# Kernel tuning notes

Hardware: AMD Instinct MI355X
Metric: run time of the kernel (lower is better)

The kernel has to match this reference:

```python
import jax, jax.numpy as jnp
import numpy as np

B, T, C, D = 4, 2048, 1024, 64

def setup_inputs() -> dict:
    key = jax.random.key(0)
    ks = jax.random.split(key, 7)
    s = 1.0 / np.sqrt(C)
    return {
        "x":  jax.random.normal(ks[0], (B, T, C), dtype=jnp.float32),
        "Wq": jax.random.uniform(ks[1], (C, D), jnp.float32, -s, s),
        "bq": jax.random.uniform(ks[2], (D,),  jnp.float32, -s, s),
        "Wk": jax.random.uniform(ks[3], (C, D), jnp.float32, -s, s),
        "bk": jax.random.uniform(ks[4], (D,),  jnp.float32, -s, s),
        "Wv": jax.random.uniform(ks[5], (C, D), jnp.float32, -s, s),
        "bv": jax.random.uniform(ks[6], (D,),  jnp.float32, -s, s),
    }

def reference(x, Wq, bq, Wk, bk, Wv, bv):
    # QKV projections: [B,T,C] @ [C,D] -> [B,T,D]
    Q = jnp.einsum('btc,cd->btd', x, Wq) + bq
    K = jnp.einsum('btc,cd->btd', x, Wk) + bk
    V = jnp.einsum('btc,cd->btd', x, Wv) + bv
    scale = 1.0 / jnp.sqrt(jnp.float32(D))
    wei = jnp.einsum('bqd,bkd->bqk', Q, K) * scale  # [B,T,T]
    causal = jnp.tril(jnp.ones((T, T), dtype=bool))
    wei = jnp.where(causal, wei, jnp.float32(-1e9))  # masked_fill, not -inf
    wei = jax.nn.softmax(wei, axis=-1)
    return jnp.einsum('bqk,bkd->bqd', wei, V)  # [B,T,D]
```

## Files before the change

kernel.cpp:

```cpp
#include <hip/hip_runtime.h>
#include <stdint.h>

#define B_  4
#define T_  2048
#define C_  1024
#define D_  64

typedef float  f32x4  __attribute__((ext_vector_type(4)));
typedef float  f32x16 __attribute__((ext_vector_type(16)));
typedef short  s16x8  __attribute__((ext_vector_type(8)));

#define QSCALE 0.18033688011112042f

static __device__ __forceinline__ uint32_t f2bf(float f) {
  uint32_t u = __builtin_bit_cast(uint32_t, f);
  u += 0x7FFFu + ((u >> 16) & 1u);
  return u >> 16;
}
static __device__ __forceinline__ uint32_t pack2bf(float a, float b) {
  return f2bf(a) | (f2bf(b) << 16);
}

__global__ __launch_bounds__(256) void wconv_kernel(
    const float* __restrict__ Wq, const float* __restrict__ bq,
    const float* __restrict__ Wk, const float* __restrict__ bk,
    const float* __restrict__ Wv, const float* __restrict__ bv,
    uint16_t* __restrict__ Wp, float* __restrict__ biascat) {
  const int g = blockIdx.x * 256 + threadIdx.x;
  const int s32   = g / 768;
  const int rem   = g - s32 * 768;
  const int ntile = rem >> 6;
  const int l     = rem & 63;
  const int mrow  = l & 15, u = l >> 4;
  const int n     = ntile * 16 + mrow;
  const int mat   = n >> 6, col = n & 63;
  const float* W  = (mat == 0) ? Wq : ((mat == 1) ? Wk : Wv);
  const float  s  = (mat == 0) ? QSCALE : 1.0f;
  const int c0    = s32 * 32 + u * 8;
  float v[8];
#pragma unroll
  for (int j = 0; j < 8; ++j) v[j] = W[(size_t)(c0 + j) * D_ + col] * s;
  uint4 st;
  st.x = pack2bf(v[0], v[1]);
  st.y = pack2bf(v[2], v[3]);
  st.z = pack2bf(v[4], v[5]);
  st.w = pack2bf(v[6], v[7]);
  *reinterpret_cast<uint4*>(Wp + (size_t)g * 8) = st;
  if (g < 192) {
    float bb;
    if (g < 64)       bb = bq[g] * QSCALE;
    else if (g < 128) bb = bk[g - 64];
    else              bb = bv[g - 128];
    biascat[g] = bb;
  }
}

__global__ __launch_bounds__(256) void proj_kernel(
    const float* __restrict__ x, const uint16_t* __restrict__ Wp,
    const float* __restrict__ biascat,
    uint16_t* __restrict__ Qfrag, uint16_t* __restrict__ Kfrag,
    uint16_t* __restrict__ Vfrag) {
  __shared__ __align__(16) uint16_t xt[2][16 * 132];
  __shared__ __align__(16) uint16_t tbuf[4][16 * 28];
  const int tid  = threadIdx.x;
  const int wave = tid >> 6;
  const int lane = tid & 63;
  const int mrow = lane & 15;
  const int u    = lane >> 4;
  const int m0   = blockIdx.x * 16;
  const int srow = tid >> 4, scol = tid & 15;

  const float* xg = x + (size_t)(m0 + srow) * C_ + scol * 4;

  f32x4 acc[3];
#pragma unroll
  for (int i = 0; i < 3; ++i)
#pragma unroll
    for (int r = 0; r < 4; ++r) acc[i][r] = 0.f;

  float4 xv0 = *reinterpret_cast<const float4*>(xg);
  float4 xv1 = *reinterpret_cast<const float4*>(xg + 64);
  {
    uint2 w0, w1;
    w0.x = pack2bf(xv0.x, xv0.y);  w0.y = pack2bf(xv0.z, xv0.w);
    w1.x = pack2bf(xv1.x, xv1.y);  w1.y = pack2bf(xv1.z, xv1.w);
    *reinterpret_cast<uint2*>(&xt[0][srow * 132 + scol * 4])      = w0;
    *reinterpret_cast<uint2*>(&xt[0][srow * 132 + scol * 4 + 64]) = w1;
  }
  __syncthreads();

  for (int s = 0; s < 8; ++s) {
    const int cur = s & 1;
    if (s < 7) {
      xv0 = *reinterpret_cast<const float4*>(xg + (s + 1) * 128);
      xv1 = *reinterpret_cast<const float4*>(xg + (s + 1) * 128 + 64);
    }
#pragma unroll
    for (int step = 0; step < 4; ++step) {
      const int s32 = s * 4 + step;
      s16x8 bf = *reinterpret_cast<const s16x8*>(
          &xt[cur][mrow * 132 + step * 32 + u * 8]);
      const uint16_t* wb = Wp + ((size_t)(s32 * 12 + wave * 3) * 64 + lane) * 8;
      s16x8 a0 = *reinterpret_cast<const s16x8*>(wb);
      s16x8 a1 = *reinterpret_cast<const s16x8*>(wb + 64 * 8);
      s16x8 a2 = *reinterpret_cast<const s16x8*>(wb + 128 * 8);
      acc[0] = __builtin_amdgcn_mfma_f32_16x16x32_bf16(a0, bf, acc[0], 0, 0, 0);
      acc[1] = __builtin_amdgcn_mfma_f32_16x16x32_bf16(a1, bf, acc[1], 0, 0, 0);
      acc[2] = __builtin_amdgcn_mfma_f32_16x16x32_bf16(a2, bf, acc[2], 0, 0, 0);
    }
    if (s < 7) {
      uint2 w0, w1;
      w0.x = pack2bf(xv0.x, xv0.y);  w0.y = pack2bf(xv0.z, xv0.w);
      w1.x = pack2bf(xv1.x, xv1.y);  w1.y = pack2bf(xv1.z, xv1.w);
      *reinterpret_cast<uint2*>(&xt[cur ^ 1][srow * 132 + scol * 4])      = w0;
      *reinterpret_cast<uint2*>(&xt[cur ^ 1][srow * 132 + scol * 4 + 64]) = w1;
      __syncthreads();
    }
  }

  const int bb  = m0 >> 11;
  const int mm  = m0 & (T_ - 1);
#pragma unroll
  for (int nt = 0; nt < 3; ++nt) {
    const int nb = wave * 48 + nt * 16;
    uint16_t vals[4];
#pragma unroll
    for (int r = 0; r < 4; ++r)
      vals[r] = (uint16_t)f2bf(acc[nt][r] + biascat[nb + u * 4 + r]);
    if (nb >= 128) {
      const int tg  = mm + mrow;
      const int t   = tg >> 5, rem = tg & 31;
      const int kc  = rem >> 4, hi2 = (rem >> 3) & 1, jj = rem & 7;
      uint16_t* base = Vfrag + ((size_t)(bb * 64 + t)) * 2048;
#pragma unroll
      for (int r = 0; r < 4; ++r) {
        int d = nb - 128 + u * 4 + r;
        int i = (d >> 5) * 2 + kc;
        int l = hi2 * 32 + (d & 31);
        base[i * 512 + l * 8 + jj] = vals[r];
      }
    } else {
#pragma unroll
      for (int r = 0; r < 4; ++r)
        tbuf[wave][mrow * 28 + u * 4 + r] = vals[r];
      const int row = lane >> 2, qtr = lane & 3;
      uint2 v = *reinterpret_cast<const uint2*>(&tbuf[wave][row * 28 + qtr * 4]);
      const int m  = m0 + row;
      const int e0 = (nb & 63) + qtr * 4;
      const int t  = (m & 2047) >> 5;
      const int c  = e0 >> 4, hi2 = (e0 >> 3) & 1, j0 = e0 & 7;
      uint16_t* dst = (nb < 64) ? Qfrag : Kfrag;
      *reinterpret_cast<uint2*>(
          dst + ((size_t)(bb * 64 + t)) * 2048 + c * 512 +
          (hi2 * 32 + (m & 31)) * 8 + j0) = v;
    }
  }
}

__global__ __launch_bounds__(256) void attn_kernel(
    const uint16_t* __restrict__ Qfrag, const uint16_t* __restrict__ Kfrag,
    const uint16_t* __restrict__ Vfrag, float* __restrict__ partial,
    float* __restrict__ lpart) {
  __shared__ float wpart[4 * 2048];
  __shared__ float lw[128];

  const int tid  = threadIdx.x;
  const int wave = tid >> 6;
  const int lane = tid & 63;
  const int ql   = lane & 31;
  const int hi   = lane >> 5;

  const int blk = blockIdx.x;
  const int b   = (blk & 7) >> 1;
  const int j   = 2 * (blk >> 3) + (blk & 1);

  int a_ = 0;
  while (8 * (a_ + 1) * (a_ + 2) <= j) ++a_;
  const int off = j - 8 * a_ * (a_ + 1);
  const int r_  = off / (a_ + 1);
  const int ch  = off - r_ * (a_ + 1);
  const int qt  = 16 * a_ + r_;
  const int c16 = ch * 16;
  const int tmax = min(c16 + 15, qt);
  const int pj  = b * 160 + j;

  s16x8 qf[4];
  {
    const uint16_t* qg = Qfrag + ((size_t)(b * 64 + qt)) * 2048 + lane * 8;
#pragma unroll
    for (int c = 0; c < 4; ++c)
      qf[c] = *reinterpret_cast<const s16x8*>(qg + c * 512);
  }

  f32x16 aco[2];
#pragma unroll
  for (int i = 0; i < 2; ++i)
#pragma unroll
    for (int r = 0; r < 16; ++r) aco[i][r] = 0.f;
  float lacc = 0.f;

  auto load_tile = [&](int t, s16x8* kf, s16x8* vf) {
    const uint16_t* kg = Kfrag + ((size_t)(b * 64 + t)) * 2048 + lane * 8;
#pragma unroll
    for (int c = 0; c < 4; ++c)
      kf[c] = *reinterpret_cast<const s16x8*>(kg + c * 512);
    const uint16_t* vg = Vfrag + ((size_t)(b * 64 + t)) * 2048 + lane * 8;
#pragma unroll
    for (int i = 0; i < 4; ++i)
      vf[i] = *reinterpret_cast<const s16x8*>(vg + i * 512);
  };

  auto compute = [&](int t, const s16x8* kf, const s16x8* vf) {
    f32x16 sacc;
#pragma unroll
    for (int r = 0; r < 16; ++r) sacc[r] = 0.f;
#pragma unroll
    for (int c = 0; c < 4; ++c)
      sacc = __builtin_amdgcn_mfma_f32_32x32x16_bf16(kf[c], qf[c], sacc, 0, 0, 0);
    if (t == qt) {
#pragma unroll
      for (int r = 0; r < 16; ++r) {
        const int koff = (r & 3) + 8 * (r >> 2) + 4 * hi;
        sacc[r] = (koff > ql) ? -1e30f : sacc[r];
      }
    }
    float p[16];
#pragma unroll
    for (int r = 0; r < 16; ++r) p[r] = __builtin_amdgcn_exp2f(sacc[r]);
    float s01 = (p[0] + p[1]) + (p[2] + p[3]);
    float s23 = (p[4] + p[5]) + (p[6] + p[7]);
    float s45 = (p[8] + p[9]) + (p[10] + p[11]);
    float s67 = (p[12] + p[13]) + (p[14] + p[15]);
    lacc += (s01 + s23) + (s45 + s67);

    uint32_t A0 = pack2bf(p[0], p[1]),  A1 = pack2bf(p[2], p[3]);
    uint32_t B0 = pack2bf(p[4], p[5]),  B1 = pack2bf(p[6], p[7]);
    uint32_t C0 = pack2bf(p[8], p[9]),  C1 = pack2bf(p[10], p[11]);
    uint32_t D0 = pack2bf(p[12], p[13]), D1 = pack2bf(p[14], p[15]);
    uint32_t r0 = (uint32_t)__shfl_xor((int)(hi ? A0 : B0), 32, 64);
    uint32_t r1 = (uint32_t)__shfl_xor((int)(hi ? A1 : B1), 32, 64);
    uint32_t r2 = (uint32_t)__shfl_xor((int)(hi ? C0 : D0), 32, 64);
    uint32_t r3 = (uint32_t)__shfl_xor((int)(hi ? C1 : D1), 32, 64);
    union { uint32_t u[4]; s16x8 v; } pf0, pf1;
    pf0.u[0] = hi ? r0 : A0;  pf0.u[1] = hi ? r1 : A1;
    pf0.u[2] = hi ? B0 : r0;  pf0.u[3] = hi ? B1 : r1;
    pf1.u[0] = hi ? r2 : C0;  pf1.u[1] = hi ? r3 : C1;
    pf1.u[2] = hi ? D0 : r2;  pf1.u[3] = hi ? D1 : r3;
    aco[0] = __builtin_amdgcn_mfma_f32_32x32x16_bf16(vf[0], pf0.v, aco[0], 0, 0, 0);
    aco[1] = __builtin_amdgcn_mfma_f32_32x32x16_bf16(vf[2], pf0.v, aco[1], 0, 0, 0);
    aco[0] = __builtin_amdgcn_mfma_f32_32x32x16_bf16(vf[1], pf1.v, aco[0], 0, 0, 0);
    aco[1] = __builtin_amdgcn_mfma_f32_32x32x16_bf16(vf[3], pf1.v, aco[1], 0, 0, 0);
  };

  {
    int t = c16 + wave;
    if (t <= tmax) {
      s16x8 kfA[4], vfA[4], kfB[4], vfB[4];
      load_tile(t, kfA, vfA);
      while (true) {
        int tn = t + 4;
        if (tn <= tmax) load_tile(tn, kfB, vfB);
        compute(t, kfA, vfA);
        if (tn > tmax) break;
        t = tn; tn = t + 4;
        if (tn <= tmax) load_tile(tn, kfA, vfA);
        compute(t, kfB, vfB);
        if (tn > tmax) break;
        t = tn;
      }
    }
  }

  lacc += __shfl_xor(lacc, 32, 64);

#pragma unroll
  for (int dm = 0; dm < 2; ++dm)
#pragma unroll
    for (int r = 0; r < 16; ++r)
      wpart[wave * 2048 + dm * 1024 + r * 64 + hi * 32 + ql] = aco[dm][r];
  if (hi == 0) lw[wave * 32 + ql] = lacc;
  __syncthreads();

  {
    const int base = tid * 8;
    float4 s0 = {0.f, 0.f, 0.f, 0.f}, s1 = {0.f, 0.f, 0.f, 0.f};
#pragma unroll
    for (int w = 0; w < 4; ++w) {
      const float* p = wpart + w * 2048 + base;
      float4 a = *reinterpret_cast<const float4*>(p);
      float4 c = *reinterpret_cast<const float4*>(p + 4);
      s0.x += a.x; s0.y += a.y; s0.z += a.z; s0.w += a.w;
      s1.x += c.x; s1.y += c.y; s1.z += c.z; s1.w += c.w;
    }
    float* pp = partial + (size_t)pj * 2048 + base;
    *reinterpret_cast<float4*>(pp)     = s0;
    *reinterpret_cast<float4*>(pp + 4) = s1;
    if (tid < 32) {
      float ls = (lw[tid] + lw[32 + tid]) + (lw[64 + tid] + lw[96 + tid]);
      lpart[(size_t)pj * 32 + tid] = ls;
    }
  }
}

__global__ __launch_bounds__(256) void reduce_kernel(
    const float* __restrict__ partial, const float* __restrict__ lpart,
    float* __restrict__ out) {
  __shared__ float trans[64 * 33];
  __shared__ float lbuf[32];
  const int blk = blockIdx.x;
  const int b   = blk >> 6;
  const int qt  = blk & 63;
  const int a_  = qt >> 4;
  const int nch = a_ + 1;
  const int pjb = b * 160 + 8 * a_ * (a_ + 1) + (qt & 15) * (a_ + 1);
  const int t   = threadIdx.x;

  if (t < 32) {
    float s = 0.f;
    for (int c = 0; c < nch; ++c) s += lpart[(size_t)(pjb + c) * 32 + t];
    lbuf[t] = 1.0f / s;
  }

  const int base = t * 8;
  float4 s0 = {0.f, 0.f, 0.f, 0.f}, s1 = {0.f, 0.f, 0.f, 0.f};
  for (int c = 0; c < nch; ++c) {
    const float* p = partial + (size_t)(pjb + c) * 2048 + base;
    float4 a = *reinterpret_cast<const float4*>(p);
    float4 d = *reinterpret_cast<const float4*>(p + 4);
    s0.x += a.x; s0.y += a.y; s0.z += a.z; s0.w += a.w;
    s1.x += d.x; s1.y += d.y; s1.z += d.z; s1.w += d.w;
  }
  const int dm = base >> 10, r = (base >> 6) & 15, hi = (base >> 5) & 1;
  const int ql0 = base & 31;
  const int d = dm * 32 + (r & 3) + 8 * (r >> 2) + 4 * hi;
  float* tr = &trans[d * 33 + ql0];
  tr[0] = s0.x; tr[1] = s0.y; tr[2] = s0.z; tr[3] = s0.w;
  tr[4] = s1.x; tr[5] = s1.y; tr[6] = s1.z; tr[7] = s1.w;
  __syncthreads();

  const int q  = t >> 3;
  const int dg = (t & 7) * 8;
  const float rinv = lbuf[q];
  float4 o0, o1;
  o0.x = trans[(dg + 0) * 33 + q] * rinv;
  o0.y = trans[(dg + 1) * 33 + q] * rinv;
  o0.z = trans[(dg + 2) * 33 + q] * rinv;
  o0.w = trans[(dg + 3) * 33 + q] * rinv;
  o1.x = trans[(dg + 4) * 33 + q] * rinv;
  o1.y = trans[(dg + 5) * 33 + q] * rinv;
  o1.z = trans[(dg + 6) * 33 + q] * rinv;
  o1.w = trans[(dg + 7) * 33 + q] * rinv;
  float* op = out + ((size_t)(b * T_ + qt * 32 + q)) * D_ + dg;
  *reinterpret_cast<float4*>(op)     = o0;
  *reinterpret_cast<float4*>(op + 4) = o1;
}

extern "C" void kernel_launch(void* const* d_in, const int* in_sizes, int n_in,
                              void* d_out, int out_size, void* d_ws, size_t ws_size,
                              hipStream_t stream) {
  (void)in_sizes; (void)n_in; (void)out_size; (void)ws_size;
  const float* x  = (const float*)d_in[0];
  const float* Wq = (const float*)d_in[1];
  const float* bq = (const float*)d_in[2];
  const float* Wk = (const float*)d_in[3];
  const float* bk = (const float*)d_in[4];
  const float* Wv = (const float*)d_in[5];
  const float* bv = (const float*)d_in[6];
  float* out = (float*)d_out;

  char* ws = (char*)d_ws;
  uint16_t* Wp      = (uint16_t*)(ws);
  float*    biascat = (float*)(ws + 393216);
  uint16_t* Qfrag   = (uint16_t*)(ws + 394240);
  uint16_t* Kfrag   = (uint16_t*)(ws + 1442816);
  uint16_t* Vfrag   = (uint16_t*)(ws + 2491392);
  float*    partial = (float*)(ws + 3539968);
  float*    lpart   = (float*)(ws + 8782848);

  hipLaunchKernelGGL(wconv_kernel, dim3(96), dim3(256), 0, stream,
                     Wq, bq, Wk, bk, Wv, bv, Wp, biascat);
  hipLaunchKernelGGL(proj_kernel, dim3(512), dim3(256), 0, stream,
                     x, Wp, biascat, Qfrag, Kfrag, Vfrag);
  hipLaunchKernelGGL(attn_kernel, dim3(640), dim3(256), 0, stream,
                     Qfrag, Kfrag, Vfrag, partial, lpart);
  hipLaunchKernelGGL(reduce_kernel, dim3(256), dim3(256), 0, stream,
                     partial, lpart, out);
}
```

Measured before the change: 105.7 us.

## Fuse attention reduction into attn kernel with 8-wave blocks per query tile

Drops the split-KV chunking (640 blocks writing partial sums to global memory plus a separate reduce kernel) and has each 512-thread block handle a whole query tile, with 8 waves striding over key tiles and reducing in shared memory before normalizing and writing output directly. This removes the partial/lpart global round trip and one kernel launch. The cost is coarser parallelism: only 256 blocks, each with a causal-length-dependent amount of work. Heavy tiles are scheduled first (qt descending) to soften the imbalance, and shared memory use doubles to about 64KB per block.

```diff
diff --git a/kernel.cpp b/kernel.cpp
--- a/kernel.cpp
+++ b/kernel.cpp
@@ -118,8 +118,8 @@
     }
   }
 
-  const int bb  = m0 >> 11;
-  const int mm  = m0 & (T_ - 1);
+  const int bb = m0 >> 11;
+  const int mm = m0 & (T_ - 1);
 #pragma unroll
   for (int nt = 0; nt < 3; ++nt) {
     const int nb = wave * 48 + nt * 16;
@@ -157,12 +157,12 @@
   }
 }
 
-__global__ __launch_bounds__(256) void attn_kernel(
+__global__ __launch_bounds__(512) void attn_kernel(
     const uint16_t* __restrict__ Qfrag, const uint16_t* __restrict__ Kfrag,
-    const uint16_t* __restrict__ Vfrag, float* __restrict__ partial,
-    float* __restrict__ lpart) {
-  __shared__ float wpart[4 * 2048];
-  __shared__ float lw[128];
+    const uint16_t* __restrict__ Vfrag, float* __restrict__ out) {
+  __shared__ float wpart[8 * 2048];
+  __shared__ float lw[8 * 32];
+  __shared__ float lbuf[32];
 
   const int tid  = threadIdx.x;
   const int wave = tid >> 6;
@@ -171,18 +171,8 @@
   const int hi   = lane >> 5;
 
   const int blk = blockIdx.x;
-  const int b   = (blk & 7) >> 1;
-  const int j   = 2 * (blk >> 3) + (blk & 1);
-
-  int a_ = 0;
-  while (8 * (a_ + 1) * (a_ + 2) <= j) ++a_;
-  const int off = j - 8 * a_ * (a_ + 1);
-  const int r_  = off / (a_ + 1);
-  const int ch  = off - r_ * (a_ + 1);
-  const int qt  = 16 * a_ + r_;
-  const int c16 = ch * 16;
-  const int tmax = min(c16 + 15, qt);
-  const int pj  = b * 160 + j;
+  const int b   = blk & 3;
+  const int qt  = 63 - (blk >> 2);
 
   s16x8 qf[4];
   {
@@ -253,19 +243,19 @@
   };
 
   {
-    int t = c16 + wave;
-    if (t <= tmax) {
+    int t = wave;
+    if (t <= qt) {
       s16x8 kfA[4], vfA[4], kfB[4], vfB[4];
       load_tile(t, kfA, vfA);
       while (true) {
-        int tn = t + 4;
-        if (tn <= tmax) load_tile(tn, kfB, vfB);
+        int tn = t + 8;
+        if (tn <= qt) load_tile(tn, kfB, vfB);
         compute(t, kfA, vfA);
-        if (tn > tmax) break;
-        t = tn; tn = t + 4;
-        if (tn <= tmax) load_tile(tn, kfA, vfA);
+        if (tn > qt) break;
+        t = tn; tn = t + 8;
+        if (tn <= qt) load_tile(tn, kfA, vfA);
         compute(t, kfB, vfB);
-        if (tn > tmax) break;
+        if (tn > qt) break;
         t = tn;
       }
     }
@@ -281,78 +271,43 @@
   if (hi == 0) lw[wave * 32 + ql] = lacc;
   __syncthreads();
 
-  {
-    const int base = tid * 8;
-    float4 s0 = {0.f, 0.f, 0.f, 0.f}, s1 = {0.f, 0.f, 0.f, 0.f};
-#pragma unroll
-    for (int w = 0; w < 4; ++w) {
-      const float* p = wpart + w * 2048 + base;
-      float4 a = *reinterpret_cast<const float4*>(p);
-      float4 c = *reinterpret_cast<const float4*>(p + 4);
-      s0.x += a.x; s0.y += a.y; s0.z += a.z; s0.w += a.w;
-      s1.x += c.x; s1.y += c.y; s1.z += c.z; s1.w += c.w;
-    }
-    float* pp = partial + (size_t)pj * 2048 + base;
-    *reinterpret_cast<float4*>(pp)     = s0;
-    *reinterpret_cast<float4*>(pp + 4) = s1;
-    if (tid < 32) {
-      float ls = (lw[tid] + lw[32 + tid]) + (lw[64 + tid] + lw[96 + tid]);
-      lpart[(size_t)pj * 32 + tid] = ls;
-    }
-  }
-}
-
-__global__ __launch_bounds__(256) void reduce_kernel(
-    const float* __restrict__ partial, const float* __restrict__ lpart,
-    float* __restrict__ out) {
-  __shared__ float trans[64 * 33];
-  __shared__ float lbuf[32];
-  const int blk = blockIdx.x;
-  const int b   = blk >> 6;
-  const int qt  = blk & 63;
-  const int a_  = qt >> 4;
-  const int nch = a_ + 1;
-  const int pjb = b * 160 + 8 * a_ * (a_ + 1) + (qt & 15) * (a_ + 1);
-  const int t   = threadIdx.x;
-
-  if (t < 32) {
-    float s = 0.f;
-    for (int c = 0; c < nch; ++c) s += lpart[(size_t)(pjb + c) * 32 + t];
-    lbuf[t] = 1.0f / s;
-  }
-
-  const int base = t * 8;
-  float4 s0 = {0.f, 0.f, 0.f, 0.f}, s1 = {0.f, 0.f, 0.f, 0.f};
-  for (int c = 0; c < nch; ++c) {
-    const float* p = partial + (size_t)(pjb + c) * 2048 + base;
-    float4 a = *reinterpret_cast<const float4*>(p);
-    float4 d = *reinterpret_cast<const float4*>(p + 4);
+  const int base = tid * 4;
+  float4 s0 = {0.f, 0.f, 0.f, 0.f};
+#pragma unroll
+  for (int w = 0; w < 8; ++w) {
+    float4 a = *reinterpret_cast<const float4*>(wpart + w * 2048 + base);
     s0.x += a.x; s0.y += a.y; s0.z += a.z; s0.w += a.w;
-    s1.x += d.x; s1.y += d.y; s1.z += d.z; s1.w += d.w;
-  }
-  const int dm = base >> 10, r = (base >> 6) & 15, hi = (base >> 5) & 1;
-  const int ql0 = base & 31;
-  const int d = dm * 32 + (r & 3) + 8 * (r >> 2) + 4 * hi;
-  float* tr = &trans[d * 33 + ql0];
-  tr[0] = s0.x; tr[1] = s0.y; tr[2] = s0.z; tr[3] = s0.w;
-  tr[4] = s1.x; tr[5] = s1.y; tr[6] = s1.z; tr[7] = s1.w;
+  }
+  if (tid < 32) {
+    float ls = 0.f;
+#pragma unroll
+    for (int w = 0; w < 8; ++w) ls += lw[w * 32 + tid];
+    lbuf[tid] = 1.0f / ls;
+  }
   __syncthreads();
 
-  const int q  = t >> 3;
-  const int dg = (t & 7) * 8;
-  const float rinv = lbuf[q];
-  float4 o0, o1;
-  o0.x = trans[(dg + 0) * 33 + q] * rinv;
-  o0.y = trans[(dg + 1) * 33 + q] * rinv;
-  o0.z = trans[(dg + 2) * 33 + q] * rinv;
-  o0.w = trans[(dg + 3) * 33 + q] * rinv;
-  o1.x = trans[(dg + 4) * 33 + q] * rinv;
-  o1.y = trans[(dg + 5) * 33 + q] * rinv;
-  o1.z = trans[(dg + 6) * 33 + q] * rinv;
-  o1.w = trans[(dg + 7) * 33 + q] * rinv;
-  float* op = out + ((size_t)(b * T_ + qt * 32 + q)) * D_ + dg;
-  *reinterpret_cast<float4*>(op)     = o0;
-  *reinterpret_cast<float4*>(op + 4) = o1;
+  float* trans = wpart;
+  {
+    const int dm = base >> 10, r = (base >> 6) & 15, h2 = (base >> 5) & 1;
+    const int ql0 = base & 31;
+    const int d = dm * 32 + (r & 3) + 8 * (r >> 2) + 4 * h2;
+    float* tr = &trans[d * 33 + ql0];
+    tr[0] = s0.x; tr[1] = s0.y; tr[2] = s0.z; tr[3] = s0.w;
+  }
+  __syncthreads();
+
+  {
+    const int q  = tid >> 4;
+    const int dg = (tid & 15) * 4;
+    const float rinv = lbuf[q];
+    float4 o;
+    o.x = trans[(dg + 0) * 33 + q] * rinv;
+    o.y = trans[(dg + 1) * 33 + q] * rinv;
+    o.z = trans[(dg + 2) * 33 + q] * rinv;
+    o.w = trans[(dg + 3) * 33 + q] * rinv;
+    *reinterpret_cast<float4*>(
+        out + ((size_t)(b * T_ + qt * 32 + q)) * D_ + dg) = o;
+  }
 }
 
 extern "C" void kernel_launch(void* const* d_in, const int* in_sizes, int n_in,
@@ -374,15 +329,11 @@
   uint16_t* Qfrag   = (uint16_t*)(ws + 394240);
   uint16_t* Kfrag   = (uint16_t*)(ws + 1442816);
   uint16_t* Vfrag   = (uint16_t*)(ws + 2491392);
-  float*    partial = (float*)(ws + 3539968);
-  float*    lpart   = (float*)(ws + 8782848);
 
   hipLaunchKernelGGL(wconv_kernel, dim3(96), dim3(256), 0, stream,
                      Wq, bq, Wk, bk, Wv, bv, Wp, biascat);
   hipLaunchKernelGGL(proj_kernel, dim3(512), dim3(256), 0, stream,
                      x, Wp, biascat, Qfrag, Kfrag, Vfrag);
-  hipLaunchKernelGGL(attn_kernel, dim3(640), dim3(256), 0, stream,
-                     Qfrag, Kfrag, Vfrag, partial, lpart);
-  hipLaunchKernelGGL(reduce_kernel, dim3(256), dim3(256), 0, stream,
-                     partial, lpart, out);
-}
+  hipLaunchKernelGGL(attn_kernel, dim3(256), dim3(512), 0, stream,
+                     Qfrag, Kfrag, Vfrag, out);
+}
```

Measured after the change: 101.5 us (median of 2 runs). 4.0% less time.
